# Kernel optimization log

Measured on AMD Instinct MI355X. Metric: run time of the kernel, lower is better.

## Reference

```python
import jax, jax.numpy as jnp
import numpy as np

NUM_HEADS = 32
HEAD_DIM = 64
ROPE_THETA = 10000.0


def _rope_cos_sin(position_ids, head_dim, theta):
    # inv_freq: [head_dim/2]
    half = head_dim // 2
    inv_freq = 1.0 / (theta ** (jnp.arange(0, half, dtype=jnp.float32) * 2.0 / head_dim))
    angles = position_ids.astype(jnp.float32)[..., None] * inv_freq  # [B,S,half]
    return jnp.cos(angles), jnp.sin(angles)


def _apply_rope(x, cos, sin):
    # x: [B,S,H,hd]; cos/sin: [B,S,half] -> broadcast over heads (rotate-half, Llama style)
    half = x.shape[-1] // 2
    x1, x2 = x[..., :half], x[..., half:]
    c = cos[:, :, None, :]
    s = sin[:, :, None, :]
    return jnp.concatenate([x1 * c - x2 * s, x2 * c + x1 * s], axis=-1)


def setup_inputs() -> dict:
    key = jax.random.key(0)
    ks = jax.random.split(key, 8)
    B, S, D = 2, 2048, 2048
    hidden_states = jax.random.normal(ks[0], (B, S, D), dtype=jnp.float32)
    # causal additive mask (is_causal=False in IpexSDP; mask carries causality)
    causal = jnp.tril(jnp.ones((S, S), dtype=jnp.bool_))
    attention_mask = jnp.where(causal, 0.0, -1e9).astype(jnp.float32)[None, None, :, :]
    attention_mask = jnp.broadcast_to(attention_mask, (B, 1, S, S))
    position_ids = jnp.broadcast_to(jnp.arange(S, dtype=jnp.int64)[None, :], (B, S))
    scale = 0.02
    qkv_w = jax.random.normal(ks[1], (3, D, D), dtype=jnp.float32) * scale
    qkv_b = jax.random.normal(ks[2], (3, D), dtype=jnp.float32) * scale
    o_w = jax.random.normal(ks[3], (D, D), dtype=jnp.float32) * scale
    o_b = jax.random.normal(ks[4], (D,), dtype=jnp.float32) * scale
    residual = jax.random.normal(ks[5], (B, S, D), dtype=jnp.float32)
    return {
        'hidden_states': hidden_states,
        'attention_mask': attention_mask,
        'position_ids': position_ids,
        'qkv_w': qkv_w,
        'qkv_b': qkv_b,
        'o_w': o_w,
        'o_b': o_b,
        'residual': residual,
    }


def reference(hidden_states, attention_mask, position_ids, qkv_w, qkv_b, o_w, o_b, residual):
    B, S, D = hidden_states.shape
    H, hd = NUM_HEADS, HEAD_DIM
    # fused QKV projection (weights stored transposed: x @ W), matching mm_qkv_out
    qkv = jnp.einsum('bsd,tde->tbse', hidden_states, qkv_w) + qkv_b[:, None, None, :]
    q = qkv[0].reshape(B, S, H, hd)
    k = qkv[1].reshape(B, S, H, hd)
    v = qkv[2].reshape(B, S, H, hd)
    cos, sin = _rope_cos_sin(position_ids, hd, ROPE_THETA)
    q = _apply_rope(q, cos, sin)
    k = _apply_rope(k, cos, sin)
    scale = 1.0 / jnp.sqrt(jnp.asarray(hd, dtype=hidden_states.dtype))
    # [B,H,S,S]
    scores = jnp.einsum('bqhd,bkhd->bhqk', q, k) * scale + attention_mask
    probs = jax.nn.softmax(scores, axis=-1)
    attn = jnp.einsum('bhqk,bkhd->bqhd', probs, v).reshape(B, S, D)
    # o-proj fused with bias + residual add (matmul_add_add)
    out = attn @ o_w + o_b + residual
    return out
```

## Files before the change

### kernel.cpp

```cpp
#include <hip/hip_runtime.h>
#include <stdint.h>
#include <stdio.h>

#define D_MODEL 2048
#define SEQ     2048
#define NHEADS  32
#define HDIM    64
#define BATCH   2
#define BH      (BATCH * NHEADS)
#define GK      2048
#define NT      (GK / 64)

typedef unsigned short u16;
typedef unsigned int   u32;
typedef __attribute__((ext_vector_type(8))) short short8;
typedef __attribute__((ext_vector_type(4))) short s16x4;
typedef __attribute__((ext_vector_type(4))) float f32x4;
typedef __attribute__((ext_vector_type(4))) u32   u32x4;
typedef __attribute__((ext_vector_type(2))) u32   u32x2;

__device__ __forceinline__ float bf2f(u16 x) {
  union { u32 u; float f; } c; c.u = ((u32)x) << 16; return c.f;
}
__device__ __forceinline__ u16 f2bf(float f) {
  union { float f; u32 u; } c; c.f = f;
  u32 u = c.u;
  return (u16)((u + 0x7FFFu + ((u >> 16) & 1u)) >> 16);
}
__device__ __forceinline__ u32 fbits(float f) {
  union { float f; u32 u; } c; c.f = f; return c.u;
}

typedef const __attribute__((address_space(1))) u32* gas_t;
typedef __attribute__((address_space(3))) u32* las_t;
__device__ __forceinline__ void gll16(const void* g, void* l) {
  __builtin_amdgcn_global_load_lds((gas_t)g, (las_t)l, 16, 0, 0);
}
__device__ __forceinline__ u32 lds_addr(const void* p) {
  return (u32)(size_t)(const __attribute__((address_space(3))) void*)p;
}
template <int OFF>
__device__ __forceinline__ short8 ds_read128o(u32 addr) {
  short8 r;
  asm volatile("ds_read_b128 %0, %1 offset:%2" : "=v"(r) : "v"(addr), "i"(OFF));
  return r;
}

#define SBAR0 __builtin_amdgcn_sched_barrier(0)

__device__ __forceinline__ void swiz_mn(int pid, int nx, int& mtile, int& ntile) {
  int chunk = 8 * nx;
  int grp = pid / chunk, loc = pid - grp * chunk;
  mtile = grp * 8 + (loc & 7);
  ntile = loc >> 3;
}

__global__ __launch_bounds__(256) void cvt_k(const float* __restrict__ in,
                                             u16* __restrict__ out) {
  int id = blockIdx.x * 256 + threadIdx.x;
  f32x4 v = *(const f32x4*)&in[(size_t)id * 4];
  alignas(8) u16 o[4];
#pragma unroll
  for (int j = 0; j < 4; j++) o[j] = f2bf(v[j]);
  *(u32x2*)&out[(size_t)id * 4] = *(const u32x2*)o;
}

__global__ __launch_bounds__(256) void transpose_cvt_k(const float* __restrict__ qkv_w,
                                                       const float* __restrict__ o_w,
                                                       u16* __restrict__ outT) {
  __shared__ u16 tile[64][72];
  const int z = blockIdx.z;
  const float* inz = (z < 3) ? qkv_w + (size_t)z * D_MODEL * D_MODEL : o_w;
  u16* outz = outT + (size_t)z * D_MODEL * D_MODEL;
  const int r0 = blockIdx.y * 64, c0 = blockIdx.x * 64;
  const int t = threadIdx.x;
  const int lrow = t >> 4, lcol4 = (t & 15) * 4;
#pragma unroll
  for (int i = 0; i < 4; i++) {
    int r = lrow + i * 16;
    f32x4 v = *(const f32x4*)&inz[(size_t)(r0 + r) * D_MODEL + (c0 + lcol4)];
#pragma unroll
    for (int j = 0; j < 4; j++) tile[r][lcol4 + j] = f2bf(v[j]);
  }
  __syncthreads();
  const int row = t >> 3, col8 = (t & 7) * 8;
#pragma unroll
  for (int i = 0; i < 2; i++) {
    int r = row + i * 32;
    alignas(16) u16 vals[8];
#pragma unroll
    for (int j = 0; j < 8; j++) vals[j] = tile[col8 + j][r];
    *(u32x4*)&outz[(size_t)(c0 + r) * D_MODEL + (r0 + col8)] = *(const u32x4*)vals;
  }
}


__device__ __forceinline__ void stage_half(const u16* __restrict__ src, int rowbase, int k0,
                                           u16* tile, int h, int w, int srl, int scol) {
  u16* ldsb = tile + h * (128 * 64);
  const u16* g0 = &src[(size_t)(rowbase + h * 128 + srl) * GK + k0 + scol];
  const u16* g1 = &src[(size_t)(rowbase + h * 128 + srl + 8) * GK + k0 + scol];
  gll16(g0, (char*)ldsb + w * 2048);
  gll16(g1, (char*)ldsb + w * 2048 + 1024);
}

__device__ __forceinline__ void rd8(short8 dst[4][2], u32 base, u32 cq0, u32 cq1) {
  u32 b0 = base + cq0, b1 = base + cq1;
  dst[0][0] = ds_read128o<0>(b0);    dst[0][1] = ds_read128o<0>(b1);
  dst[1][0] = ds_read128o<2048>(b0); dst[1][1] = ds_read128o<2048>(b1);
  dst[2][0] = ds_read128o<4096>(b0); dst[2][1] = ds_read128o<4096>(b1);
  dst[3][0] = ds_read128o<6144>(b0); dst[3][1] = ds_read128o<6144>(b1);
}

template <int NFLO>
__device__ __forceinline__ void mfma_half(const short8 afc[4][2], const short8 bfc[4][2],
                                          f32x4 acc[4][4]) {
  __builtin_amdgcn_s_setprio(1);
#pragma unroll
  for (int mf = 0; mf < 4; mf++)
#pragma unroll
    for (int nf = NFLO; nf < NFLO + 2; nf++) {
      acc[mf][nf] = __builtin_amdgcn_mfma_f32_16x16x32_bf16(afc[mf][0], bfc[nf][0], acc[mf][nf], 0, 0, 0);
      acc[mf][nf] = __builtin_amdgcn_mfma_f32_16x16x32_bf16(afc[mf][1], bfc[nf][1], acc[mf][nf], 0, 0, 0);
    }
  __builtin_amdgcn_s_setprio(0);
}

#define KT_BODY(KT_, AFC, BFC, AFN, BFN)                                        \
  do {                                                                           \
    if ((KT_) + 1 < NT) rd8(AFN, asb + (u32)ri * (u32)(128 * 64 * 2) + rowA, cq0, cq1); \
    if ((KT_) + 1 < NT) { asm volatile("s_waitcnt lgkmcnt(8)"); }                \
    else                { asm volatile("s_waitcnt lgkmcnt(0)"); }                \
    SBAR0;                                                                       \
    mfma_half<0>(AFC, BFC, acc);                                                 \
    if ((KT_) + 1 < NT) rd8(BFN, bsb + (u32)ri * (u32)(256 * 64 * 2) + rowB, cq0, cq1); \
    SBAR0;                                                                       \
    mfma_half<2>(AFC, BFC, acc);                                                 \
    __builtin_amdgcn_s_barrier();                                                \
    SBAR0;                                                                       \
    if ((KT_) + 3 < NT) {                                                        \
      const int k3_ = ((KT_) + 3) * 64;                                          \
      stage_half(Ag, m0, k3_, AsB + si * (128 * 64), 0, w, srl, scol);           \
      stage_half(Bg, n0, k3_, BsB + si * (256 * 64), 0, w, srl, scol);           \
      stage_half(Bg, n0, k3_, BsB + si * (256 * 64), 1, w, srl, scol);           \
      asm volatile("s_waitcnt vmcnt(6)");                                        \
    } else {                                                                     \
      asm volatile("s_waitcnt vmcnt(0)");                                        \
    }                                                                            \
    SBAR0;                                                                       \
    __builtin_amdgcn_s_barrier();                                                \
    SBAR0;                                                                       \
    { int th_ = 3 - si - ri; si = ri; ri = th_; }                                \
  } while (0)

__device__ __forceinline__ void gemm_128x256(const u16* __restrict__ Ag,
                                             const u16* __restrict__ Bg,
                                             int m0, int n0,
                                             u16* AsB, u16* BsB,
                                             f32x4 acc[4][4]) {
  const int t = threadIdx.x, w = t >> 6, lane = t & 63;
  const int quad = lane >> 4, l16 = lane & 15;
  const int wr = w >> 2, wc = w & 3;
  const int srl = w * 16 + (lane >> 3);
  const int scol = (((lane & 7) ^ (lane >> 3)) << 3);
  const u32 asb = lds_addr(AsB), bsb = lds_addr(BsB);
  const u32 xorc = (u32)((l16 & 7) << 4);
  const u32 cq0 = (u32)(quad * 16) ^ xorc;
  const u32 cq1 = (u32)(64 + quad * 16) ^ xorc;
  const u32 rowA = (u32)((wr * 64 + l16) * 128);
  const u32 rowB = (u32)((wc * 64 + l16) * 128);

#pragma unroll
  for (int mf = 0; mf < 4; mf++)
#pragma unroll
    for (int nf = 0; nf < 4; nf++)
#pragma unroll
      for (int i = 0; i < 4; i++) acc[mf][nf][i] = 0.0f;

#pragma unroll
  for (int tt = 0; tt < 3; tt++) {
    stage_half(Ag, m0, tt * 64, AsB + tt * (128 * 64), 0, w, srl, scol);
    stage_half(Bg, n0, tt * 64, BsB + tt * (256 * 64), 0, w, srl, scol);
    stage_half(Bg, n0, tt * 64, BsB + tt * (256 * 64), 1, w, srl, scol);
  }
  asm volatile("s_waitcnt vmcnt(6)");
  SBAR0;
  __builtin_amdgcn_s_barrier();
  SBAR0;

  short8 af0[4][2], bf0[4][2], af1[4][2], bf1[4][2];
  rd8(af0, asb + rowA, cq0, cq1);
  rd8(bf0, bsb + rowB, cq0, cq1);
  int si = 0, ri = 1;

  for (int kt = 0; kt < NT; kt += 2) {
    KT_BODY(kt,     af0, bf0, af1, bf1);
    KT_BODY(kt + 1, af1, bf1, af0, bf0);
  }
}

__global__ __launch_bounds__(512, 1) void qkv_gemm_k(const u16* __restrict__ A,
                                                     const u16* __restrict__ BT,
                                                     const float* __restrict__ bias,
                                                     u16* __restrict__ Qb, u16* __restrict__ Kb,
                                                     u16* __restrict__ Vbt) {
  __shared__ u16 As[3][128 * 64];
  __shared__ u16 Bs[3][256 * 64];
  f32x4 acc[4][4];
  int mtile, ntile;
  swiz_mn(blockIdx.x, 24, mtile, ntile);
  const int m0 = mtile * 128, n0 = ntile * 256;
  gemm_128x256(A, BT, m0, n0, &As[0][0], &Bs[0][0], acc);

  const int t = threadIdx.x, lane = t & 63, quad = lane >> 4, l16 = lane & 15;
  const int w = t >> 6, wr = w >> 2, wc = w & 3;
  const int tsel = n0 >> 11;
  if (tsel < 2) {
    u16* dst = tsel ? Kb : Qb;
#pragma unroll
    for (int p = 0; p < 2; p++) {
      int nlo = n0 + wc * 64 + p * 16 + l16;
      float blo = bias[nlo], bhi = bias[nlo + 32];
      int j = p * 16 + l16;
      float inv = __expf((float)j * -0.28782313662425572f);
      int h = (nlo & 2047) >> 6;
#pragma unroll
      for (int mf = 0; mf < 4; mf++) {
#pragma unroll
        for (int r = 0; r < 4; r++) {
          int m = m0 + wr * 64 + mf * 16 + quad * 4 + r;
          int b = m >> 11, s = m & (SEQ - 1);
          float sn, cs;
          __sincosf((float)s * inv, &sn, &cs);
          float x1 = acc[mf][p][r] + blo;
          float x2 = acc[mf][p + 2][r] + bhi;
          size_t base = ((size_t)((b * NHEADS + h) * SEQ + s)) * HDIM;
          dst[base + j]      = f2bf(x1 * cs - x2 * sn);
          dst[base + j + 32] = f2bf(x2 * cs + x1 * sn);
        }
      }
    }
  } else {
#pragma unroll
    for (int nf = 0; nf < 4; nf++) {
      int n = n0 + wc * 64 + nf * 16 + l16;
      float bv = bias[n];
      int e = n & 2047, h = e >> 6, d = e & 63;
#pragma unroll
      for (int mf = 0; mf < 4; mf++) {
        int m0r = m0 + wr * 64 + mf * 16 + quad * 4;
        int b = m0r >> 11, s0 = m0r & (SEQ - 1);
        alignas(8) u16 o4[4];
#pragma unroll
        for (int r = 0; r < 4; r++) o4[r] = f2bf(acc[mf][nf][r] + bv);
        *(u32x2*)&Vbt[((size_t)((b * NHEADS + h) * HDIM + d)) * SEQ + s0] = *(const u32x2*)o4;
      }
    }
  }
}

__global__ __launch_bounds__(512, 1) void oproj_gemm_k(const u16* __restrict__ A,
                                                       const u16* __restrict__ BT,
                                                       const float* __restrict__ bias,
                                                       const float* __restrict__ resid,
                                                       float* __restrict__ out) {
  __shared__ u16 As[3][128 * 64];
  __shared__ u16 Bs[3][256 * 64];
  f32x4 acc[4][4];
  int mtile, ntile;
  swiz_mn(blockIdx.x, 8, mtile, ntile);
  const int m0 = mtile * 128, n0 = ntile * 256;
  gemm_128x256(A, BT, m0, n0, &As[0][0], &Bs[0][0], acc);

  const int t = threadIdx.x, lane = t & 63, quad = lane >> 4, l16 = lane & 15;
  const int w = t >> 6, wr = w >> 2, wc = w & 3;
#pragma unroll
  for (int nf = 0; nf < 4; nf++) {
    int n = n0 + wc * 64 + nf * 16 + l16;
    float bv = bias[n];
#pragma unroll
    for (int mf = 0; mf < 4; mf++) {
#pragma unroll
      for (int r = 0; r < 4; r++) {
        int m = m0 + wr * 64 + mf * 16 + quad * 4 + r;
        size_t oi = (size_t)m * D_MODEL + n;
        out[oi] = acc[mf][nf][r] + bv + resid[oi];
      }
    }
  }
}

__global__ __launch_bounds__(256, 2) void attn_k(const u16* __restrict__ Qb,
                                                 const u16* __restrict__ Kb,
                                                 const u16* __restrict__ Vbt,
                                                 u16* __restrict__ attn) {
  __shared__ u16 smem[128 * 72];
  u16* Ks = smem;
  u16* Vt = smem + 64 * 72;
  const int blk = blockIdx.x;
  const int bh = blk & 63, pi = blk >> 6;
  const int b = bh >> 5, h = bh & 31;
  const int t = threadIdx.x, w = t >> 6, lane = t & 63, quad = lane >> 4, l16 = lane & 15;
  const int qbT[2] = { pi * 128, (15 - pi) * 128 };
  const int qwT[2] = { qbT[0] + w * 32, qbT[1] + w * 32 };
  const size_t bho = (size_t)bh * SEQ * HDIM;
  const size_t vbo = (size_t)bh * HDIM * SEQ;
  const int kend = qbT[1] + 128;

  short8 qf[2][2][2];
#pragma unroll
  for (int Ti = 0; Ti < 2; Ti++)
#pragma unroll
    for (int qt = 0; qt < 2; qt++)
#pragma unroll
      for (int kd = 0; kd < 2; kd++) {
        short8 v = *(const short8*)&Qb[bho + (size_t)(qwT[Ti] + qt * 16 + l16) * HDIM + kd * 32 + quad * 8];
#pragma unroll
        for (int i = 0; i < 8; i++) {
          float f = bf2f((u16)v[i]) * 0.125f;
          v[i] = (short)f2bf(f);
        }
        qf[Ti][qt][kd] = v;
      }

  f32x4 Oacc[2][4][2];
  float mrow[2][2] = {{-1e30f, -1e30f}, {-1e30f, -1e30f}};
  float lrow[2][2] = {{0.0f, 0.0f}, {0.0f, 0.0f}};
#pragma unroll
  for (int Ti = 0; Ti < 2; Ti++)
#pragma unroll
    for (int dt = 0; dt < 4; dt++)
#pragma unroll
      for (int qt = 0; qt < 2; qt++)
#pragma unroll
        for (int i = 0; i < 4; i++) Oacc[Ti][dt][qt][i] = 0.0f;

  const int srow = t >> 3, sc8 = (t & 7) * 8;
  u32x4 kreg[2], vreg[2];

#pragma unroll
  for (int j = 0; j < 2; j++) {
    kreg[j] = *(const u32x4*)&Kb[bho + (size_t)(srow + j * 32) * HDIM + sc8];
    vreg[j] = *(const u32x4*)&Vbt[vbo + (size_t)(srow + j * 32) * SEQ + sc8];
  }
#pragma unroll
  for (int j = 0; j < 2; j++) {
    *(u32x4*)&Ks[(srow + j * 32) * 72 + sc8] = kreg[j];
    *(u32x4*)&Vt[(srow + j * 32) * 72 + sc8] = vreg[j];
  }
  __syncthreads();

  for (int key0 = 0; key0 < kend; key0 += 64) {
    const int nxt = key0 + 64;
    if (nxt < kend) {
#pragma unroll
      for (int j = 0; j < 2; j++) {
        kreg[j] = *(const u32x4*)&Kb[bho + (size_t)(nxt + srow + j * 32) * HDIM + sc8];
        vreg[j] = *(const u32x4*)&Vbt[vbo + (size_t)(srow + j * 32) * SEQ + nxt + sc8];
      }
    }
#pragma unroll
    for (int Ti = 0; Ti < 2; Ti++) {
      const int qw = qwT[Ti];
      if (key0 <= qw + 31) {
        const int lim = qw + 31 - key0;
        int nkt = (lim >> 4) + 1; if (nkt > 4) nkt = 4;
        f32x4 sacc[4][2];
#pragma unroll
        for (int kt = 0; kt < 4; kt++) {
          if (kt < nkt) {
            short8 kf0 = *(const short8*)&Ks[(kt * 16 + l16) * 72 + quad * 8];
            short8 kf1 = *(const short8*)&Ks[(kt * 16 + l16) * 72 + 32 + quad * 8];
#pragma unroll
            for (int qt = 0; qt < 2; qt++) {
              f32x4 z = {0.0f, 0.0f, 0.0f, 0.0f};
              z = __builtin_amdgcn_mfma_f32_16x16x32_bf16(kf0, qf[Ti][qt][0], z, 0, 0, 0);
              z = __builtin_amdgcn_mfma_f32_16x16x32_bf16(kf1, qf[Ti][qt][1], z, 0, 0, 0);
              sacc[kt][qt] = z;
            }
          }
        }
        if (key0 + 63 > qw) {
#pragma unroll
          for (int qt = 0; qt < 2; qt++) {
            int qrow = qw + qt * 16 + l16;
#pragma unroll
            for (int kt = 0; kt < 4; kt++)
              if (kt < nkt)
#pragma unroll
                for (int r = 0; r < 4; r++)
                  if (key0 + kt * 16 + quad * 4 + r > qrow) sacc[kt][qt][r] = -1e30f;
          }
        }
        float alpha[2];
#pragma unroll
        for (int qt = 0; qt < 2; qt++) {
          float mx = -1e30f;
#pragma unroll
          for (int kt = 0; kt < 4; kt++)
            if (kt < nkt)
#pragma unroll
              for (int r = 0; r < 4; r++) mx = fmaxf(mx, sacc[kt][qt][r]);
          mx = fmaxf(mx, __shfl_xor(mx, 16));
          mx = fmaxf(mx, __shfl_xor(mx, 32));
          float mnew = fmaxf(mrow[Ti][qt], mx);
          alpha[qt] = __expf(mrow[Ti][qt] - mnew);
          mrow[Ti][qt] = mnew;
          float rsum = 0.0f;
#pragma unroll
          for (int kt = 0; kt < 4; kt++)
            if (kt < nkt)
#pragma unroll
              for (int r = 0; r < 4; r++) {
                float pv = __expf(sacc[kt][qt][r] - mnew);
                sacc[kt][qt][r] = pv;
                rsum += pv;
              }
          rsum += __shfl_xor(rsum, 16);
          rsum += __shfl_xor(rsum, 32);
          lrow[Ti][qt] = lrow[Ti][qt] * alpha[qt] + rsum;
        }
#pragma unroll
        for (int dt = 0; dt < 4; dt++)
#pragma unroll
          for (int qt = 0; qt < 2; qt++)
#pragma unroll
            for (int r = 0; r < 4; r++) Oacc[Ti][dt][qt][r] *= alpha[qt];
#pragma unroll
        for (int kt = 0; kt < 4; kt++) {
          if (kt < nkt) {
            s16x4 pk[2];
#pragma unroll
            for (int qt = 0; qt < 2; qt++) {
              u32 a0 = fbits(sacc[kt][qt][0]) + 0x8000u;
              u32 a1 = fbits(sacc[kt][qt][1]) + 0x8000u;
              u32 a2 = fbits(sacc[kt][qt][2]) + 0x8000u;
              u32 a3 = fbits(sacc[kt][qt][3]) + 0x8000u;
              union { u32 u[2]; s16x4 s; } pc;
              pc.u[0] = __builtin_amdgcn_perm(a1, a0, 0x07060302u);
              pc.u[1] = __builtin_amdgcn_perm(a3, a2, 0x07060302u);
              pk[qt] = pc.s;
            }
            s16x4 vf[4];
#pragma unroll
            for (int dt = 0; dt < 4; dt++)
              vf[dt] = *(const s16x4*)&Vt[(dt * 16 + l16) * 72 + kt * 16 + quad * 4];
#pragma unroll
            for (int dt = 0; dt < 4; dt++)
#pragma unroll
              for (int qt = 0; qt < 2; qt++)
                Oacc[Ti][dt][qt] = __builtin_amdgcn_mfma_f32_16x16x16bf16_1k(vf[dt], pk[qt], Oacc[Ti][dt][qt], 0, 0, 0);
          }
        }
      }
    }
    __syncthreads();
    if (nxt < kend) {
#pragma unroll
      for (int j = 0; j < 2; j++) {
        *(u32x4*)&Ks[(srow + j * 32) * 72 + sc8] = kreg[j];
        *(u32x4*)&Vt[(srow + j * 32) * 72 + sc8] = vreg[j];
      }
      __syncthreads();
    }
  }

#pragma unroll
  for (int Ti = 0; Ti < 2; Ti++) {
    float invl[2] = {1.0f / lrow[Ti][0], 1.0f / lrow[Ti][1]};
#pragma unroll
    for (int dt = 0; dt < 4; dt++)
#pragma unroll
      for (int qt = 0; qt < 2; qt++)
#pragma unroll
        for (int r = 0; r < 4; r++)
          smem[(w * 32 + qt * 16 + l16) * 72 + dt * 16 + quad * 4 + r] =
              f2bf(Oacc[Ti][dt][qt][r] * invl[qt]);
    __syncthreads();
#pragma unroll
    for (int ii = 0; ii < 4; ii++) {
      int chunk = t + ii * 256;
      int row = chunk >> 3, g = chunk & 7;
      *(u32x4*)&attn[((size_t)(b * SEQ + qbT[Ti] + row)) * D_MODEL + h * 64 + g * 8] =
          *(const u32x4*)&smem[row * 72 + g * 8];
    }
    __syncthreads();
  }
}

extern "C" void kernel_launch(void* const* d_in, const int* in_sizes, int n_in,
                              void* d_out, int out_size, void* d_ws, size_t ws_size,
                              hipStream_t stream) {
  (void)in_sizes; (void)n_in; (void)out_size;
  const float* hidden = (const float*)d_in[0];
  const float* qkv_w = (const float*)d_in[3];
  const float* qkv_b = (const float*)d_in[4];
  const float* o_w   = (const float*)d_in[5];
  const float* o_b   = (const float*)d_in[6];
  const float* resid = (const float*)d_in[7];
  float* out = (float*)d_out;

  u16* ws = (u16*)d_ws;
  size_t off = 0;
  u16* hidb  = ws + off; off += (size_t)BATCH * SEQ * D_MODEL;
  u16* qkvT  = ws + off; off += (size_t)3 * D_MODEL * D_MODEL;
  u16* owT   = ws + off; off += (size_t)D_MODEL * D_MODEL;
  u16* Qb    = ws + off; off += (size_t)BH * SEQ * HDIM;
  u16* Kb    = ws + off; off += (size_t)BH * SEQ * HDIM;
  u16* Vbt   = ws + off; off += (size_t)BH * SEQ * HDIM;
  u16* attnb = ws + off; off += (size_t)BATCH * SEQ * D_MODEL;
  if (ws_size < off * sizeof(u16)) {
    fprintf(stderr, "kernel_launch: workspace too small: need %zu bytes, have %zu\n",
            off * sizeof(u16), ws_size);
    return;
  }
  (void)owT;

  cvt_k<<<(BATCH * SEQ * D_MODEL) / (4 * 256), 256, 0, stream>>>(hidden, hidb);
  transpose_cvt_k<<<dim3(32, 32, 4), 256, 0, stream>>>(qkv_w, o_w, qkvT);
  qkv_gemm_k<<<32 * 24, 512, 0, stream>>>(hidb, qkvT, qkv_b, Qb, Kb, Vbt);
  attn_k<<<BH * 8, 256, 0, stream>>>(Qb, Kb, Vbt, attnb);
  oproj_gemm_k<<<32 * 8, 512, 0, stream>>>(attnb, owT, o_b, resid, out);
}
```

Baseline: 415.6 us.

## Double-buffer attention K/V tiles in LDS with 128-key stages

```diff
diff --git a/kernel.cpp b/kernel.cpp
--- a/kernel.cpp
+++ b/kernel.cpp
@@ -93,7 +93,6 @@
     *(u32x4*)&outz[(size_t)(c0 + r) * D_MODEL + (r0 + col8)] = *(const u32x4*)vals;
   }
 }
-
 
 __device__ __forceinline__ void stage_half(const u16* __restrict__ src, int rowbase, int k0,
                                            u16* tile, int h, int w, int srl, int scol) {
@@ -290,13 +289,13 @@
   }
 }
 
+#define ATT_BUF (128 * 72 + 64 * 136)
+
 __global__ __launch_bounds__(256, 2) void attn_k(const u16* __restrict__ Qb,
                                                  const u16* __restrict__ Kb,
                                                  const u16* __restrict__ Vbt,
                                                  u16* __restrict__ attn) {
-  __shared__ u16 smem[128 * 72];
-  u16* Ks = smem;
-  u16* Vt = smem + 64 * 72;
+  __shared__ u16 smem[2 * ATT_BUF];
   const int blk = blockIdx.x;
   const int bh = blk & 63, pi = blk >> 6;
   const int b = bh >> 5, h = bh & 31;
@@ -306,6 +305,7 @@
   const size_t bho = (size_t)bh * SEQ * HDIM;
   const size_t vbo = (size_t)bh * HDIM * SEQ;
   const int kend = qbT[1] + 128;
+  const int nr = kend >> 7;
 
   short8 qf[2][2][2];
 #pragma unroll
@@ -335,134 +335,152 @@
 #pragma unroll
         for (int i = 0; i < 4; i++) Oacc[Ti][dt][qt][i] = 0.0f;
 
-  const int srow = t >> 3, sc8 = (t & 7) * 8;
-  u32x4 kreg[2], vreg[2];
-
-#pragma unroll
-  for (int j = 0; j < 2; j++) {
-    kreg[j] = *(const u32x4*)&Kb[bho + (size_t)(srow + j * 32) * HDIM + sc8];
-    vreg[j] = *(const u32x4*)&Vbt[vbo + (size_t)(srow + j * 32) * SEQ + sc8];
-  }
-#pragma unroll
-  for (int j = 0; j < 2; j++) {
-    *(u32x4*)&Ks[(srow + j * 32) * 72 + sc8] = kreg[j];
-    *(u32x4*)&Vt[(srow + j * 32) * 72 + sc8] = vreg[j];
+  const int krow = t >> 3, kcol = (t & 7) * 8;
+  u32x4 kreg[4], vreg[4];
+
+#pragma unroll
+  for (int c = 0; c < 4; c++) {
+    kreg[c] = *(const u32x4*)&Kb[bho + (size_t)(krow + c * 32) * HDIM + kcol];
+    int id = t + c * 256, vrow = id >> 4, vcol = (id & 15) * 8;
+    vreg[c] = *(const u32x4*)&Vbt[vbo + (size_t)vrow * SEQ + vcol];
+  }
+  {
+    u16* Ks = smem;
+    u16* Vt = smem + 128 * 72;
+#pragma unroll
+    for (int c = 0; c < 4; c++) {
+      *(u32x4*)&Ks[(krow + c * 32) * 72 + kcol] = kreg[c];
+      int id = t + c * 256, vrow = id >> 4, vcol = (id & 15) * 8;
+      *(u32x4*)&Vt[vrow * 136 + vcol] = vreg[c];
+    }
   }
   __syncthreads();
 
-  for (int key0 = 0; key0 < kend; key0 += 64) {
-    const int nxt = key0 + 64;
-    if (nxt < kend) {
-#pragma unroll
-      for (int j = 0; j < 2; j++) {
-        kreg[j] = *(const u32x4*)&Kb[bho + (size_t)(nxt + srow + j * 32) * HDIM + sc8];
-        vreg[j] = *(const u32x4*)&Vbt[vbo + (size_t)(srow + j * 32) * SEQ + nxt + sc8];
-      }
-    }
-#pragma unroll
-    for (int Ti = 0; Ti < 2; Ti++) {
-      const int qw = qwT[Ti];
-      if (key0 <= qw + 31) {
-        const int lim = qw + 31 - key0;
-        int nkt = (lim >> 4) + 1; if (nkt > 4) nkt = 4;
-        f32x4 sacc[4][2];
-#pragma unroll
-        for (int kt = 0; kt < 4; kt++) {
-          if (kt < nkt) {
-            short8 kf0 = *(const short8*)&Ks[(kt * 16 + l16) * 72 + quad * 8];
-            short8 kf1 = *(const short8*)&Ks[(kt * 16 + l16) * 72 + 32 + quad * 8];
+  for (int r = 0; r < nr; r++) {
+    const int key0 = r << 7;
+    const int cur = r & 1;
+    u16* Ks = smem + cur * ATT_BUF;
+    u16* Vt = Ks + 128 * 72;
+    if (r + 1 < nr) {
+      const int nk0 = key0 + 128;
+#pragma unroll
+      for (int c = 0; c < 4; c++) {
+        kreg[c] = *(const u32x4*)&Kb[bho + (size_t)(nk0 + krow + c * 32) * HDIM + kcol];
+        int id = t + c * 256, vrow = id >> 4, vcol = (id & 15) * 8;
+        vreg[c] = *(const u32x4*)&Vbt[vbo + (size_t)vrow * SEQ + nk0 + vcol];
+      }
+    }
+#pragma unroll
+    for (int s = 0; s < 2; s++) {
+      const int k0s = key0 + s * 64;
+      const int so = s * 64;
+#pragma unroll
+      for (int Ti = 0; Ti < 2; Ti++) {
+        const int qw = qwT[Ti];
+        if (k0s <= qw + 31) {
+          const int lim = qw + 31 - k0s;
+          int nkt = (lim >> 4) + 1; if (nkt > 4) nkt = 4;
+          f32x4 sacc[4][2];
+#pragma unroll
+          for (int kt = 0; kt < 4; kt++) {
+            if (kt < nkt) {
+              short8 kf0 = *(const short8*)&Ks[(so + kt * 16 + l16) * 72 + quad * 8];
+              short8 kf1 = *(const short8*)&Ks[(so + kt * 16 + l16) * 72 + 32 + quad * 8];
+#pragma unroll
+              for (int qt = 0; qt < 2; qt++) {
+                f32x4 z = {0.0f, 0.0f, 0.0f, 0.0f};
+                z = __builtin_amdgcn_mfma_f32_16x16x32_bf16(kf0, qf[Ti][qt][0], z, 0, 0, 0);
+                z = __builtin_amdgcn_mfma_f32_16x16x32_bf16(kf1, qf[Ti][qt][1], z, 0, 0, 0);
+                sacc[kt][qt] = z;
+              }
+            }
+          }
+          if (k0s + 63 > qw) {
 #pragma unroll
             for (int qt = 0; qt < 2; qt++) {
-              f32x4 z = {0.0f, 0.0f, 0.0f, 0.0f};
-              z = __builtin_amdgcn_mfma_f32_16x16x32_bf16(kf0, qf[Ti][qt][0], z, 0, 0, 0);
-              z = __builtin_amdgcn_mfma_f32_16x16x32_bf16(kf1, qf[Ti][qt][1], z, 0, 0, 0);
-              sacc[kt][qt] = z;
+              int qrow = qw + qt * 16 + l16;
+#pragma unroll
+              for (int kt = 0; kt < 4; kt++)
+                if (kt < nkt)
+#pragma unroll
+                  for (int rr = 0; rr < 4; rr++)
+                    if (k0s + kt * 16 + quad * 4 + rr > qrow) sacc[kt][qt][rr] = -1e30f;
+            }
+          }
+          float alpha[2];
+#pragma unroll
+          for (int qt = 0; qt < 2; qt++) {
+            float mx = -1e30f;
+#pragma unroll
+            for (int kt = 0; kt < 4; kt++)
+              if (kt < nkt)
+#pragma unroll
+                for (int rr = 0; rr < 4; rr++) mx = fmaxf(mx, sacc[kt][qt][rr]);
+            mx = fmaxf(mx, __shfl_xor(mx, 16));
+            mx = fmaxf(mx, __shfl_xor(mx, 32));
+            float mnew = fmaxf(mrow[Ti][qt], mx);
+            alpha[qt] = __expf(mrow[Ti][qt] - mnew);
+            mrow[Ti][qt] = mnew;
+            float rsum = 0.0f;
+#pragma unroll
+            for (int kt = 0; kt < 4; kt++)
+              if (kt < nkt)
+#pragma unroll
+                for (int rr = 0; rr < 4; rr++) {
+                  float pv = __expf(sacc[kt][qt][rr] - mnew);
+                  sacc[kt][qt][rr] = pv;
+                  rsum += pv;
+                }
+            rsum += __shfl_xor(rsum, 16);
+            rsum += __shfl_xor(rsum, 32);
+            lrow[Ti][qt] = lrow[Ti][qt] * alpha[qt] + rsum;
+          }
+#pragma unroll
+          for (int dt = 0; dt < 4; dt++)
+#pragma unroll
+            for (int qt = 0; qt < 2; qt++)
+#pragma unroll
+              for (int rr = 0; rr < 4; rr++) Oacc[Ti][dt][qt][rr] *= alpha[qt];
+#pragma unroll
+          for (int kt = 0; kt < 4; kt++) {
+            if (kt < nkt) {
+              s16x4 pk[2];
+#pragma unroll
+              for (int qt = 0; qt < 2; qt++) {
+                u32 a0 = fbits(sacc[kt][qt][0]) + 0x8000u;
+                u32 a1 = fbits(sacc[kt][qt][1]) + 0x8000u;
+                u32 a2 = fbits(sacc[kt][qt][2]) + 0x8000u;
+                u32 a3 = fbits(sacc[kt][qt][3]) + 0x8000u;
+                union { u32 u[2]; s16x4 s; } pc;
+                pc.u[0] = __builtin_amdgcn_perm(a1, a0, 0x07060302u);
+                pc.u[1] = __builtin_amdgcn_perm(a3, a2, 0x07060302u);
+                pk[qt] = pc.s;
+              }
+              s16x4 vf[4];
+#pragma unroll
+              for (int dt = 0; dt < 4; dt++)
+                vf[dt] = *(const s16x4*)&Vt[(dt * 16 + l16) * 136 + so + kt * 16 + quad * 4];
+#pragma unroll
+              for (int dt = 0; dt < 4; dt++)
+#pragma unroll
+                for (int qt = 0; qt < 2; qt++)
+                  Oacc[Ti][dt][qt] = __builtin_amdgcn_mfma_f32_16x16x16bf16_1k(vf[dt], pk[qt], Oacc[Ti][dt][qt], 0, 0, 0);
             }
           }
         }
-        if (key0 + 63 > qw) {
-#pragma unroll
-          for (int qt = 0; qt < 2; qt++) {
-            int qrow = qw + qt * 16 + l16;
-#pragma unroll
-            for (int kt = 0; kt < 4; kt++)
-              if (kt < nkt)
-#pragma unroll
-                for (int r = 0; r < 4; r++)
-                  if (key0 + kt * 16 + quad * 4 + r > qrow) sacc[kt][qt][r] = -1e30f;
-          }
-        }
-        float alpha[2];
-#pragma unroll
-        for (int qt = 0; qt < 2; qt++) {
-          float mx = -1e30f;
-#pragma unroll
-          for (int kt = 0; kt < 4; kt++)
-            if (kt < nkt)
-#pragma unroll
-              for (int r = 0; r < 4; r++) mx = fmaxf(mx, sacc[kt][qt][r]);
-          mx = fmaxf(mx, __shfl_xor(mx, 16));
-          mx = fmaxf(mx, __shfl_xor(mx, 32));
-          float mnew = fmaxf(mrow[Ti][qt], mx);
-          alpha[qt] = __expf(mrow[Ti][qt] - mnew);
-          mrow[Ti][qt] = mnew;
-          float rsum = 0.0f;
-#pragma unroll
-          for (int kt = 0; kt < 4; kt++)
-            if (kt < nkt)
-#pragma unroll
-              for (int r = 0; r < 4; r++) {
-                float pv = __expf(sacc[kt][qt][r] - mnew);
-                sacc[kt][qt][r] = pv;
-                rsum += pv;
-              }
-          rsum += __shfl_xor(rsum, 16);
-          rsum += __shfl_xor(rsum, 32);
-          lrow[Ti][qt] = lrow[Ti][qt] * alpha[qt] + rsum;
-        }
-#pragma unroll
-        for (int dt = 0; dt < 4; dt++)
-#pragma unroll
-          for (int qt = 0; qt < 2; qt++)
-#pragma unroll
-            for (int r = 0; r < 4; r++) Oacc[Ti][dt][qt][r] *= alpha[qt];
-#pragma unroll
-        for (int kt = 0; kt < 4; kt++) {
-          if (kt < nkt) {
-            s16x4 pk[2];
-#pragma unroll
-            for (int qt = 0; qt < 2; qt++) {
-              u32 a0 = fbits(sacc[kt][qt][0]) + 0x8000u;
-              u32 a1 = fbits(sacc[kt][qt][1]) + 0x8000u;
-              u32 a2 = fbits(sacc[kt][qt][2]) + 0x8000u;
-              u32 a3 = fbits(sacc[kt][qt][3]) + 0x8000u;
-              union { u32 u[2]; s16x4 s; } pc;
-              pc.u[0] = __builtin_amdgcn_perm(a1, a0, 0x07060302u);
-              pc.u[1] = __builtin_amdgcn_perm(a3, a2, 0x07060302u);
-              pk[qt] = pc.s;
-            }
-            s16x4 vf[4];
-#pragma unroll
-            for (int dt = 0; dt < 4; dt++)
-              vf[dt] = *(const s16x4*)&Vt[(dt * 16 + l16) * 72 + kt * 16 + quad * 4];
-#pragma unroll
-            for (int dt = 0; dt < 4; dt++)
-#pragma unroll
-              for (int qt = 0; qt < 2; qt++)
-                Oacc[Ti][dt][qt] = __builtin_amdgcn_mfma_f32_16x16x16bf16_1k(vf[dt], pk[qt], Oacc[Ti][dt][qt], 0, 0, 0);
-          }
-        }
+      }
+    }
+    if (r + 1 < nr) {
+      u16* Ksn = smem + (cur ^ 1) * ATT_BUF;
+      u16* Vtn = Ksn + 128 * 72;
+#pragma unroll
+      for (int c = 0; c < 4; c++) {
+        *(u32x4*)&Ksn[(krow + c * 32) * 72 + kcol] = kreg[c];
+        int id = t + c * 256, vrow = id >> 4, vcol = (id & 15) * 8;
+        *(u32x4*)&Vtn[vrow * 136 + vcol] = vreg[c];
       }
     }
     __syncthreads();
-    if (nxt < kend) {
-#pragma unroll
-      for (int j = 0; j < 2; j++) {
-        *(u32x4*)&Ks[(srow + j * 32) * 72 + sc8] = kreg[j];
-        *(u32x4*)&Vt[(srow + j * 32) * 72 + sc8] = vreg[j];
-      }
-      __syncthreads();
-    }
   }
 
 #pragma unroll
@@ -473,9 +491,9 @@
 #pragma unroll
       for (int qt = 0; qt < 2; qt++)
 #pragma unroll
-        for (int r = 0; r < 4; r++)
-          smem[(w * 32 + qt * 16 + l16) * 72 + dt * 16 + quad * 4 + r] =
-              f2bf(Oacc[Ti][dt][qt][r] * invl[qt]);
+        for (int rr = 0; rr < 4; rr++)
+          smem[(w * 32 + qt * 16 + l16) * 72 + dt * 16 + quad * 4 + rr] =
+              f2bf(Oacc[Ti][dt][qt][rr] * invl[qt]);
     __syncthreads();
 #pragma unroll
     for (int ii = 0; ii < 4; ii++) {
```

New measurement: 412.4 us. No clear change (-0.8%).
